# Kernel tuning notes

Hardware: AMD Instinct MI355X
Metric: run time of the kernel (lower is better)

Reference implementation:

```python
import jax, jax.numpy as jnp
import numpy as np

D_IN = 1024
D_OUT = 1024
NUM_HEADS = 16
HEAD_DIM = D_OUT // NUM_HEADS


def setup_inputs() -> dict:
    key = jax.random.key(0)
    k_x, k_q, k_k, k_v, k_o, k_ob = jax.random.split(key, 6)
    s_in = 1.0 / np.sqrt(D_IN)
    s_out = 1.0 / np.sqrt(D_OUT)
    return {
        "x": jax.random.normal(k_x, (2, 2048, D_IN), dtype=jnp.float32),
        "W_q": jax.random.uniform(k_q, (D_IN, D_OUT), minval=-s_in, maxval=s_in, dtype=jnp.float32),
        "W_k": jax.random.uniform(k_k, (D_IN, D_OUT), minval=-s_in, maxval=s_in, dtype=jnp.float32),
        "W_v": jax.random.uniform(k_v, (D_IN, D_OUT), minval=-s_in, maxval=s_in, dtype=jnp.float32),
        "W_out": jax.random.uniform(k_o, (D_OUT, D_OUT), minval=-s_out, maxval=s_out, dtype=jnp.float32),
        "b_out": jax.random.uniform(k_ob, (D_OUT,), minval=-s_out, maxval=s_out, dtype=jnp.float32),
    }


def reference(x, W_q, W_k, W_v, W_out, b_out):
    b, t, _ = x.shape
    # projections (qkv_bias=False)
    q = (x @ W_q).reshape(b, t, NUM_HEADS, HEAD_DIM).transpose(0, 2, 1, 3)  # [b,h,t,d]
    k = (x @ W_k).reshape(b, t, NUM_HEADS, HEAD_DIM).transpose(0, 2, 1, 3)
    v = (x @ W_v).reshape(b, t, NUM_HEADS, HEAD_DIM).transpose(0, 2, 1, 3)
    scale = 1.0 / np.sqrt(HEAD_DIM).astype(np.float32)
    scores = jnp.einsum("bhqd,bhkd->bhqk", q, k) * scale  # [b,h,t,t]
    causal = jnp.triu(jnp.ones((t, t), dtype=bool), k=1)
    scores = jnp.where(causal, -jnp.inf, scores)
    weights = jax.nn.softmax(scores, axis=-1)
    # dropout p=0.0 -> identity
    context = jnp.einsum("bhqk,bhkd->bhqd", weights, v)
    context = context.transpose(0, 2, 1, 3).reshape(b, t, D_OUT)
    return context @ W_out + b_out
```

## Files before the change

### kernel.cpp

```cpp
#include <hip/hip_runtime.h>
#include <hip/hip_bf16.h>

#define B_  2
#define T_  2048
#define D_  1024
#define H_  16
#define DH_ 64
#define M_  (B_*T_)

typedef _Float16 f16;
typedef __attribute__((ext_vector_type(4))) _Float16 f16x4;
typedef __attribute__((ext_vector_type(8))) _Float16 f16x8;
typedef __attribute__((ext_vector_type(4))) float f32x4;

#define GLOAD_LDS(gp, lp) __builtin_amdgcn_global_load_lds( \
    (const __attribute__((address_space(1))) void*)(gp),    \
    (__attribute__((address_space(3))) void*)(lp), 16, 0, 0)

__global__ void prep(const float* __restrict__ x,
                     const float* __restrict__ wq, const float* __restrict__ wk,
                     const float* __restrict__ wv, const float* __restrict__ wo,
                     f16* __restrict__ xb, f16* __restrict__ wqkvT, f16* __restrict__ woutT) {
  __shared__ float tile[32][33];
  const int bid = blockIdx.x;
  if (bid < 2048) {
    size_t i = ((size_t)bid * 256 + threadIdx.x) * 8;
    float4 a = *(const float4*)(x + i);
    float4 b = *(const float4*)(x + i + 4);
    f16x8 o;
    o[0]=(f16)a.x; o[1]=(f16)a.y; o[2]=(f16)a.z; o[3]=(f16)a.w;
    o[4]=(f16)b.x; o[5]=(f16)b.y; o[6]=(f16)b.z; o[7]=(f16)b.w;
    *(f16x8*)(xb + i) = o;
  } else {
    const int b2 = bid - 2048;
    const int j = b2 >> 10, rem = b2 & 1023;
    const float* src = (j==0)?wq:(j==1)?wk:(j==2)?wv:wo;
    f16* dst = (j<3) ? (wqkvT + (size_t)j*D_*D_) : woutT;
    const int n0 = (rem & 31)*32, k0 = (rem >> 5)*32;
    const int tx = threadIdx.x & 31, ty = threadIdx.x >> 5;
    #pragma unroll
    for (int i=0;i<32;i+=8)
      tile[ty+i][tx] = src[(size_t)(k0+ty+i)*D_ + n0+tx];
    __syncthreads();
    #pragma unroll
    for (int i=0;i<32;i+=8)
      dst[(size_t)(n0+ty+i)*D_ + k0+tx] = (f16)tile[tx][ty+i];
  }
}

__launch_bounds__(256, 2)
__global__ void qkv_gemm(const f16* __restrict__ xb, const f16* __restrict__ wT,
                         f16* __restrict__ Qp, f16* __restrict__ Kp, f16* __restrict__ Vtp) {
  const int fid = blockIdx.x;
  const int g = fid & 7, r = fid >> 3;
  const int m0 = ((((r & 3) << 3) | g)) * 128;
  const int n0 = ((r >> 2) & 7) * 128;
  const int j  = r >> 5;
  const f16* B0 = wT + (size_t)j * D_ * D_;
  __shared__ alignas(16) char smem[65536];
  f16* AsF = (f16*)smem;
  f16* BsF = AsF + 2*128*64;
  const int tid = threadIdx.x;
  const int lane = tid & 63, wave = tid >> 6;
  const int ln = lane & 15, quad = lane >> 4;
  const int wm = wave >> 1, wn = wave & 1;

  f32x4 acc[4][4];
  #pragma unroll
  for (int a=0;a<4;++a)
    #pragma unroll
    for (int b=0;b<4;++b) acc[a][b] = f32x4{0.f,0.f,0.f,0.f};

  const bool swapped = (j < 2);
  const int slot_row[4] = { (0*256+tid)>>3, (1*256+tid)>>3, (2*256+tid)>>3, (3*256+tid)>>3 };

  #pragma unroll
  for (int p = 0; p < 4; ++p) {
    int slot = p*256 + tid;
    int row  = slot_row[p];
    int c    = (slot & 7) ^ (row & 7);
    GLOAD_LDS(xb + (size_t)(m0+row)*D_ + c*8, AsF + (size_t)slot*8);
    GLOAD_LDS(B0 + (size_t)(n0+row)*D_ + c*8, BsF + (size_t)slot*8);
  }
  __syncthreads();

  for (int it = 0; it < 16; ++it) {
    const f16* Ac = AsF + (it & 1)*8192;
    const f16* Bc = BsF + (it & 1)*8192;
    if (it < 15) {
      const int k1 = (it + 1) * 64;
      f16* An = AsF + ((it + 1) & 1)*8192;
      f16* Bn = BsF + ((it + 1) & 1)*8192;
      #pragma unroll
      for (int p = 0; p < 4; ++p) {
        int slot = p*256 + tid;
        int row  = slot_row[p];
        int c    = (slot & 7) ^ (row & 7);
        GLOAD_LDS(xb + (size_t)(m0+row)*D_ + k1 + c*8, An + (size_t)slot*8);
        GLOAD_LDS(B0 + (size_t)(n0+row)*D_ + k1 + c*8, Bn + (size_t)slot*8);
      }
    }
    #pragma unroll
    for (int ks = 0; ks < 2; ++ks) {
      const int cb = ((ks*4 + quad) ^ (ln & 7)) * 8;
      f16x8 af[4], bf[4];
      #pragma unroll
      for (int mt = 0; mt < 4; ++mt)
        af[mt] = *(const f16x8*)(Ac + (size_t)(wm*64 + mt*16 + ln)*64 + cb);
      #pragma unroll
      for (int nt = 0; nt < 4; ++nt)
        bf[nt] = *(const f16x8*)(Bc + (size_t)(wn*64 + nt*16 + ln)*64 + cb);
      if (swapped) {
        #pragma unroll
        for (int nt = 0; nt < 4; ++nt)
          #pragma unroll
          for (int mt = 0; mt < 4; ++mt)
            acc[nt][mt] = __builtin_amdgcn_mfma_f32_16x16x32_f16(bf[nt], af[mt], acc[nt][mt], 0, 0, 0);
      } else {
        #pragma unroll
        for (int mt = 0; mt < 4; ++mt)
          #pragma unroll
          for (int nt = 0; nt < 4; ++nt)
            acc[mt][nt] = __builtin_amdgcn_mfma_f32_16x16x32_f16(af[mt], bf[nt], acc[mt][nt], 0, 0, 0);
      }
    }
    __syncthreads();
  }

  if (swapped) {
    const float scale = (j == 0) ? (0.125f * 1.44269504088896f) : 1.0f;
    f16* dstB = (j == 0) ? Qp : Kp;
    #pragma unroll
    for (int nt = 0; nt < 4; ++nt)
      #pragma unroll
      for (int mt = 0; mt < 4; ++mt) {
        int gm = m0 + wm*64 + mt*16 + ln;
        int gn = n0 + wn*64 + nt*16 + quad*4;
        int bb = gm >> 11, t = gm & (T_-1);
        int h  = gn >> 6,  dd = gn & (DH_-1);
        f16x4 v;
        #pragma unroll
        for (int rr = 0; rr < 4; ++rr) v[rr] = (f16)(acc[nt][mt][rr] * scale);
        *(f16x4*)&dstB[((((size_t)bb*H_ + h)*T_ + t)*DH_) + dd] = v;
      }
  } else {
    f16* VtS = (f16*)smem;
    #pragma unroll
    for (int mt = 0; mt < 4; ++mt)
      #pragma unroll
      for (int nt = 0; nt < 4; ++nt) {
        f16x4 v;
        v[0]=(f16)acc[mt][nt][0]; v[1]=(f16)acc[mt][nt][1];
        v[2]=(f16)acc[mt][nt][2]; v[3]=(f16)acc[mt][nt][3];
        *(f16x4*)&VtS[(size_t)(wn*64 + nt*16 + ln)*136 + wm*64 + mt*16 + quad*4] = v;
      }
    __syncthreads();
    int dd_loc = tid >> 1, half = tid & 1;
    int gn = n0 + dd_loc, h = gn >> 6, dd = gn & (DH_-1);
    int bb = m0 >> 11, tb = (m0 & (T_-1)) + half*64;
    f16* dst = Vtp + ((size_t)(bb*H_ + h)*DH_ + dd)*T_ + tb;
    const f16* src = VtS + (size_t)dd_loc*136 + half*64;
    #pragma unroll
    for (int u = 0; u < 8; ++u)
      *(uint4*)(dst + u*8) = *(const uint4*)(src + u*8);
  }
}

__launch_bounds__(256, 3)
__global__ void flash(const f16* __restrict__ Qp, const f16* __restrict__ Kp,
                      const f16* __restrict__ Vtp, f16* __restrict__ ctx) {
  const int fid = blockIdx.x;
  const int bh = fid & 31;
  const int qt = 31 - (fid >> 5);
  const int b = bh >> 4, h = bh & (H_-1);
  const f16* Kh = Kp  + (size_t)bh * T_ * DH_;
  const f16* Vh = Vtp + (size_t)bh * DH_ * T_;
  const f16* Qh = Qp  + (size_t)bh * T_ * DH_;
  const int tid = threadIdx.x, lane = tid & 63, w = tid >> 6;
  const int ln = lane & 15, quad = lane >> 4;

  __shared__ alignas(16) char smem[32768];
  f16* Ks = (f16*)smem;
  f16* Vs = (f16*)(smem + 16384);

  f16x8 qf[4][2];
  #pragma unroll
  for (int g = 0; g < 4; ++g)
    #pragma unroll
    for (int ks = 0; ks < 2; ++ks)
      qf[g][ks] = *(const f16x8*)&Qh[(size_t)(qt*64 + g*16 + ln)*DH_ + ks*32 + quad*8];

  f32x4 o[4][4];
  #pragma unroll
  for (int dt = 0; dt < 4; ++dt)
    #pragma unroll
    for (int g = 0; g < 4; ++g) o[dt][g] = f32x4{0.f,0.f,0.f,0.f};
  float lp[4] = {0.f, 0.f, 0.f, 0.f};

  #pragma unroll
  for (int i = 0; i < 2; ++i) {
    int slot = i*256 + tid;
    int row  = slot >> 3;
    int c    = (slot & 7) ^ (row & 7);
    GLOAD_LDS(Kh + (size_t)row*DH_ + c*8, Ks + (size_t)slot*8);
    GLOAD_LDS(Vh + (size_t)row*T_  + c*8, Vs + (size_t)slot*8);
  }
  __syncthreads();

  for (int it = 0; it <= qt; ++it) {
    const f16* Kc = Ks + (it & 1)*4096;
    const f16* Vc = Vs + (it & 1)*4096;
    if (it < qt) {
      const int kv1 = (it + 1)*64;
      f16* Kn = Ks + ((it + 1) & 1)*4096;
      f16* Vn = Vs + ((it + 1) & 1)*4096;
      #pragma unroll
      for (int i = 0; i < 2; ++i) {
        int slot = i*256 + tid;
        int row  = slot >> 3;
        int c    = (slot & 7) ^ (row & 7);
        GLOAD_LDS(Kh + (size_t)(kv1 + row)*DH_ + c*8, Kn + (size_t)slot*8);
        GLOAD_LDS(Vh + (size_t)row*T_ + kv1 + c*8,    Vn + (size_t)slot*8);
      }
    }

    f32x4 s[4];
    #pragma unroll
    for (int g = 0; g < 4; ++g) s[g] = f32x4{0.f,0.f,0.f,0.f};
    #pragma unroll
    for (int ks = 0; ks < 2; ++ks) {
      f16x8 kx = *(const f16x8*)(Kc + (size_t)(w*16 + ln)*64 + (((ks*4 + quad) ^ (ln & 7))*8));
      #pragma unroll
      for (int g = 0; g < 4; ++g)
        s[g] = __builtin_amdgcn_mfma_f32_16x16x32_f16(kx, qf[g][ks], s[g], 0, 0, 0);
    }

    if (it == qt) {
      #pragma unroll
      for (int g = 0; g < 4; ++g)
        #pragma unroll
        for (int rr = 0; rr < 4; ++rr)
          if (w*16 + quad*4 + rr > g*16 + ln) s[g][rr] = -INFINITY;
    }

    f16x4 pb[4];
    #pragma unroll
    for (int g = 0; g < 4; ++g) {
      #pragma unroll
      for (int rr = 0; rr < 4; ++rr) {
        float pe = __builtin_amdgcn_exp2f(s[g][rr]);
        lp[g] += pe;
        pb[g][rr] = (f16)pe;
      }
    }

    #pragma unroll
    for (int dt = 0; dt < 4; ++dt) {
      f16x4 vf = *(const f16x4*)(Vc + (size_t)(dt*16 + ln)*64
                   + (((2*w + (quad >> 1)) ^ (ln & 7))*8) + (quad & 1)*4);
      #pragma unroll
      for (int g = 0; g < 4; ++g)
        o[dt][g] = __builtin_amdgcn_mfma_f32_16x16x16f16(vf, pb[g], o[dt][g], 0, 0, 0);
    }
    __syncthreads();
  }

  #pragma unroll
  for (int g = 0; g < 4; ++g) {
    lp[g] += __shfl_xor(lp[g], 16, 64);
    lp[g] += __shfl_xor(lp[g], 32, 64);
  }

  float* buf = (float*)smem;
  #define WR_PART() do {                                                        \
    _Pragma("unroll")                                                           \
    for (int dt = 0; dt < 4; ++dt)                                              \
      _Pragma("unroll")                                                         \
      for (int g = 0; g < 4; ++g)                                               \
        *(f32x4*)&buf[(size_t)(g*16 + ln)*68 + dt*16 + quad*4] = o[dt][g];      \
    if (quad == 0) {                                                            \
      _Pragma("unroll")                                                         \
      for (int g = 0; g < 4; ++g) buf[64*68 + g*16 + ln] = lp[g];               \
    }                                                                           \
  } while (0)
  #define ACC_PART() do {                                                       \
    _Pragma("unroll")                                                           \
    for (int dt = 0; dt < 4; ++dt)                                              \
      _Pragma("unroll")                                                         \
      for (int g = 0; g < 4; ++g) {                                             \
        f32x4 v = *(const f32x4*)&buf[(size_t)(g*16 + ln)*68 + dt*16 + quad*4]; \
        o[dt][g][0] += v[0]; o[dt][g][1] += v[1];                               \
        o[dt][g][2] += v[2]; o[dt][g][3] += v[3];                               \
      }                                                                         \
    _Pragma("unroll")                                                           \
    for (int g = 0; g < 4; ++g) lp[g] += buf[64*68 + g*16 + ln];                \
  } while (0)

  if (w == 1) WR_PART();
  __syncthreads();
  if (w == 0) ACC_PART();
  __syncthreads();
  if (w == 2) WR_PART();
  __syncthreads();
  if (w == 0) ACC_PART();
  __syncthreads();
  if (w == 3) WR_PART();
  __syncthreads();
  if (w == 0) ACC_PART();
  __syncthreads();
  if (w == 0) WR_PART();
  __syncthreads();

  {
    const int q  = tid >> 2;
    const int dc = (tid & 3) << 4;
    const float linv = 1.0f / buf[64*68 + q];
    const float* src = &buf[(size_t)q*68 + dc];
    f16x8 o0, o1;
    #pragma unroll
    for (int jj = 0; jj < 8; ++jj) {
      o0[jj] = (f16)(src[jj] * linv);
      o1[jj] = (f16)(src[8 + jj] * linv);
    }
    f16* dst = &ctx[(size_t)(b*T_ + qt*64 + q)*D_ + h*DH_ + dc];
    *(f16x8*)dst       = o0;
    *(f16x8*)(dst + 8) = o1;
  }
  #undef WR_PART
  #undef ACC_PART
}

__launch_bounds__(256, 2)
__global__ void out_gemm(const f16* __restrict__ ctx, const f16* __restrict__ woT,
                         const float* __restrict__ bo, float* __restrict__ out) {
  const int fid = blockIdx.x;
  const int g = fid & 7, r = fid >> 3;
  const int m0 = ((((r & 3) << 3) | g)) * 128;
  const int n0 = (r >> 2) * 128;
  __shared__ alignas(16) f16 smem[4*128*64];
  f16* AsF = smem;
  f16* BsF = AsF + 2*128*64;
  const int tid = threadIdx.x;
  const int lane = tid & 63, wave = tid >> 6;
  const int ln = lane & 15, quad = lane >> 4;
  const int wm = wave >> 1, wn = wave & 1;

  f32x4 acc[4][4];
  #pragma unroll
  for (int a=0;a<4;++a)
    #pragma unroll
    for (int b=0;b<4;++b) acc[a][b] = f32x4{0.f,0.f,0.f,0.f};

  #pragma unroll
  for (int p = 0; p < 4; ++p) {
    int slot = p*256 + tid;
    int row  = slot >> 3;
    int c    = (slot & 7) ^ (row & 7);
    GLOAD_LDS(ctx + (size_t)(m0+row)*D_ + c*8, AsF + (size_t)slot*8);
    GLOAD_LDS(woT + (size_t)(n0+row)*D_ + c*8, BsF + (size_t)slot*8);
  }
  __syncthreads();

  for (int it = 0; it < 16; ++it) {
    const f16* Ac = AsF + (it & 1)*8192;
    const f16* Bc = BsF + (it & 1)*8192;
    if (it < 15) {
      const int k1 = (it + 1) * 64;
      f16* An = AsF + ((it + 1) & 1)*8192;
      f16* Bn = BsF + ((it + 1) & 1)*8192;
      #pragma unroll
      for (int p = 0; p < 4; ++p) {
        int slot = p*256 + tid;
        int row  = slot >> 3;
        int c    = (slot & 7) ^ (row & 7);
        GLOAD_LDS(ctx + (size_t)(m0+row)*D_ + k1 + c*8, An + (size_t)slot*8);
        GLOAD_LDS(woT + (size_t)(n0+row)*D_ + k1 + c*8, Bn + (size_t)slot*8);
      }
    }
    #pragma unroll
    for (int ks = 0; ks < 2; ++ks) {
      const int cb = ((ks*4 + quad) ^ (ln & 7)) * 8;
      f16x8 af[4], bf[4];
      #pragma unroll
      for (int mt = 0; mt < 4; ++mt)
        af[mt] = *(const f16x8*)(Ac + (size_t)(wm*64 + mt*16 + ln)*64 + cb);
      #pragma unroll
      for (int nt = 0; nt < 4; ++nt)
        bf[nt] = *(const f16x8*)(Bc + (size_t)(wn*64 + nt*16 + ln)*64 + cb);
      #pragma unroll
      for (int nt = 0; nt < 4; ++nt)
        #pragma unroll
        for (int mt = 0; mt < 4; ++mt)
          acc[nt][mt] = __builtin_amdgcn_mfma_f32_16x16x32_f16(bf[nt], af[mt], acc[nt][mt], 0, 0, 0);
    }
    __syncthreads();
  }

  #pragma unroll
  for (int nt = 0; nt < 4; ++nt) {
    int gn = n0 + wn*64 + nt*16 + quad*4;
    float4 bv = *(const float4*)&bo[gn];
    #pragma unroll
    for (int mt = 0; mt < 4; ++mt) {
      int gm = m0 + wm*64 + mt*16 + ln;
      float4 v;
      v.x = acc[nt][mt][0] + bv.x;
      v.y = acc[nt][mt][1] + bv.y;
      v.z = acc[nt][mt][2] + bv.z;
      v.w = acc[nt][mt][3] + bv.w;
      *(float4*)&out[(size_t)gm*D_ + gn] = v;
    }
  }
}

extern "C" void kernel_launch(void* const* d_in, const int* in_sizes, int n_in,
                              void* d_out, int out_size, void* d_ws, size_t ws_size,
                              hipStream_t stream) {
  const float* x  = (const float*)d_in[0];
  const float* wq = (const float*)d_in[1];
  const float* wk = (const float*)d_in[2];
  const float* wv = (const float*)d_in[3];
  const float* wo = (const float*)d_in[4];
  const float* bo = (const float*)d_in[5];
  float* out = (float*)d_out;

  f16* ws    = (f16*)d_ws;
  f16* xb    = ws;
  f16* wqkvT = xb    + (size_t)M_*D_;
  f16* woutT = wqkvT + (size_t)3*D_*D_;
  f16* Qb    = woutT + (size_t)D_*D_;
  f16* Kb    = Qb    + (size_t)M_*D_;
  f16* Vb    = Kb    + (size_t)M_*D_;
  f16* ctx   = Vb    + (size_t)M_*D_;

  prep<<<6144, 256, 0, stream>>>(x, wq, wk, wv, wo, xb, wqkvT, woutT);
  qkv_gemm<<<768, 256, 0, stream>>>(xb, wqkvT, Qb, Kb, Vb);
  flash<<<1024, 256, 0, stream>>>(Qb, Kb, Vb, ctx);
  out_gemm<<<256, 256, 0, stream>>>(ctx, woutT, bo, out);
}
```

Baseline: 167.5 us.

## Triple-buffer K/V tiles in flash attention with vmcnt-based waits

Moves the flash attention K/V staging from double to triple buffering, prefetching two tiles ahead. The full __syncthreads per iteration becomes a partial s_waitcnt vmcnt(4) plus a barrier, so loads for the next tile can stay in flight while the current tile is computed. This adds 16KB of LDS per block, which may cut occupancy under the 3-blocks-per-SM launch bound. Near the end it issues redundant clamped loads of the last tile to keep the vmcnt accounting uniform.

```diff
diff --git a/kernel.cpp b/kernel.cpp
--- a/kernel.cpp
+++ b/kernel.cpp
@@ -179,9 +179,23 @@
   const int tid = threadIdx.x, lane = tid & 63, w = tid >> 6;
   const int ln = lane & 15, quad = lane >> 4;
 
-  __shared__ alignas(16) char smem[32768];
+  __shared__ alignas(16) char smem[49152];
   f16* Ks = (f16*)smem;
-  f16* Vs = (f16*)(smem + 16384);
+  f16* Vs = (f16*)(smem + 24576);
+
+  #define STAGE_KV(tt, bi) do {                                              \
+    const int kvr_ = (tt)*64;                                                \
+    _Pragma("unroll")                                                        \
+    for (int i_ = 0; i_ < 2; ++i_) {                                         \
+      int slot_ = i_*256 + tid;                                              \
+      int row_  = slot_ >> 3;                                                \
+      int c_    = (slot_ & 7) ^ (row_ & 7);                                  \
+      GLOAD_LDS(Kh + (size_t)(kvr_ + row_)*DH_ + c_*8,                       \
+                Ks + (size_t)(bi)*4096 + (size_t)slot_*8);                   \
+      GLOAD_LDS(Vh + (size_t)row_*T_ + kvr_ + c_*8,                          \
+                Vs + (size_t)(bi)*4096 + (size_t)slot_*8);                   \
+    }                                                                        \
+  } while (0)
 
   f16x8 qf[4][2];
   #pragma unroll
@@ -197,32 +211,19 @@
     for (int g = 0; g < 4; ++g) o[dt][g] = f32x4{0.f,0.f,0.f,0.f};
   float lp[4] = {0.f, 0.f, 0.f, 0.f};
 
-  #pragma unroll
-  for (int i = 0; i < 2; ++i) {
-    int slot = i*256 + tid;
-    int row  = slot >> 3;
-    int c    = (slot & 7) ^ (row & 7);
-    GLOAD_LDS(Kh + (size_t)row*DH_ + c*8, Ks + (size_t)slot*8);
-    GLOAD_LDS(Vh + (size_t)row*T_  + c*8, Vs + (size_t)slot*8);
-  }
-  __syncthreads();
+  STAGE_KV(0, 0);
+  { const int t1 = (qt >= 1) ? 1 : qt; STAGE_KV(t1, 1); }
 
   for (int it = 0; it <= qt; ++it) {
-    const f16* Kc = Ks + (it & 1)*4096;
-    const f16* Vc = Vs + (it & 1)*4096;
-    if (it < qt) {
-      const int kv1 = (it + 1)*64;
-      f16* Kn = Ks + ((it + 1) & 1)*4096;
-      f16* Vn = Vs + ((it + 1) & 1)*4096;
-      #pragma unroll
-      for (int i = 0; i < 2; ++i) {
-        int slot = i*256 + tid;
-        int row  = slot >> 3;
-        int c    = (slot & 7) ^ (row & 7);
-        GLOAD_LDS(Kh + (size_t)(kv1 + row)*DH_ + c*8, Kn + (size_t)slot*8);
-        GLOAD_LDS(Vh + (size_t)row*T_ + kv1 + c*8,    Vn + (size_t)slot*8);
-      }
-    }
+    const int cur = it % 3;
+    const f16* Kc = Ks + (size_t)cur*4096;
+    const f16* Vc = Vs + (size_t)cur*4096;
+
+    asm volatile("s_waitcnt vmcnt(4)" ::: "memory");
+    __builtin_amdgcn_s_barrier();
+    asm volatile("" ::: "memory");
+
+    { const int tn = (it + 2 <= qt) ? (it + 2) : qt; STAGE_KV(tn, (it + 2) % 3); }
 
     f32x4 s[4];
     #pragma unroll
@@ -262,8 +263,11 @@
       for (int g = 0; g < 4; ++g)
         o[dt][g] = __builtin_amdgcn_mfma_f32_16x16x16f16(vf, pb[g], o[dt][g], 0, 0, 0);
     }
-    __syncthreads();
-  }
+  }
+
+  asm volatile("s_waitcnt vmcnt(0)" ::: "memory");
+  __builtin_amdgcn_s_barrier();
+  asm volatile("" ::: "memory");
 
   #pragma unroll
   for (int g = 0; g < 4; ++g) {
@@ -328,6 +332,7 @@
   }
   #undef WR_PART
   #undef ACC_PART
+  #undef STAGE_KV
 }
 
 __launch_bounds__(256, 2)
```

Result: no change. 166.2 us (-0.8%).

## Retile QKV GEMM to 256x256 blocks with 512 threads and BK=32

Applied to the files above, without the earlier changes.

The QKV projection GEMM now uses 256x256 output tiles per block with 8 waves and a K-step of 32, using a new XOR-swizzled LDS layout and a single barrier per iteration with explicit vmcnt waits. MFMA sections are wrapped in s_setprio. The V-transpose epilogue no longer goes through LDS and writes 4-element vectors straight to the transposed layout. The aim is more operand reuse per LDS byte and fewer barriers. The risks are that 192 blocks underfill the 256 CUs, and that the V stores become narrower and strided.

```diff
diff --git a/kernel.cpp b/kernel.cpp
--- a/kernel.cpp
+++ b/kernel.cpp
@@ -48,84 +48,92 @@
   }
 }
 
-__launch_bounds__(256, 2)
+__launch_bounds__(512, 2)
 __global__ void qkv_gemm(const f16* __restrict__ xb, const f16* __restrict__ wT,
                          f16* __restrict__ Qp, f16* __restrict__ Kp, f16* __restrict__ Vtp) {
   const int fid = blockIdx.x;
-  const int g = fid & 7, r = fid >> 3;
-  const int m0 = ((((r & 3) << 3) | g)) * 128;
-  const int n0 = ((r >> 2) & 7) * 128;
-  const int j  = r >> 5;
-  const f16* B0 = wT + (size_t)j * D_ * D_;
-  __shared__ alignas(16) char smem[65536];
-  f16* AsF = (f16*)smem;
-  f16* BsF = AsF + 2*128*64;
+  const int mb = fid & 15, nf = fid >> 4;
+  const int m0 = mb * 256;
+  const int n0f = nf * 256;
+  const int j  = n0f >> 10;
+  const int n0 = n0f & 1023;
+  const f16* A0 = xb + (size_t)m0*D_;
+  const f16* B0 = wT + (size_t)j*D_*D_ + (size_t)n0*D_;
+  __shared__ alignas(16) f16 smem[4*256*32];
+  f16* As = smem;
+  f16* Bs = smem + 2*256*32;
   const int tid = threadIdx.x;
   const int lane = tid & 63, wave = tid >> 6;
   const int ln = lane & 15, quad = lane >> 4;
-  const int wm = wave >> 1, wn = wave & 1;
-
-  f32x4 acc[4][4];
+  const int wm = wave >> 2, wn = wave & 3;
+
+  const bool swapped = (j < 2);
+
+  f32x4 acc[4][8];
   #pragma unroll
   for (int a=0;a<4;++a)
     #pragma unroll
-    for (int b=0;b<4;++b) acc[a][b] = f32x4{0.f,0.f,0.f,0.f};
-
-  const bool swapped = (j < 2);
-  const int slot_row[4] = { (0*256+tid)>>3, (1*256+tid)>>3, (2*256+tid)>>3, (3*256+tid)>>3 };
-
-  #pragma unroll
-  for (int p = 0; p < 4; ++p) {
-    int slot = p*256 + tid;
-    int row  = slot_row[p];
-    int c    = (slot & 7) ^ (row & 7);
-    GLOAD_LDS(xb + (size_t)(m0+row)*D_ + c*8, AsF + (size_t)slot*8);
-    GLOAD_LDS(B0 + (size_t)(n0+row)*D_ + c*8, BsF + (size_t)slot*8);
-  }
-  __syncthreads();
-
-  for (int it = 0; it < 16; ++it) {
-    const f16* Ac = AsF + (it & 1)*8192;
-    const f16* Bc = BsF + (it & 1)*8192;
-    if (it < 15) {
-      const int k1 = (it + 1) * 64;
-      f16* An = AsF + ((it + 1) & 1)*8192;
-      f16* Bn = BsF + ((it + 1) & 1)*8192;
-      #pragma unroll
-      for (int p = 0; p < 4; ++p) {
-        int slot = p*256 + tid;
-        int row  = slot_row[p];
-        int c    = (slot & 7) ^ (row & 7);
-        GLOAD_LDS(xb + (size_t)(m0+row)*D_ + k1 + c*8, An + (size_t)slot*8);
-        GLOAD_LDS(B0 + (size_t)(n0+row)*D_ + k1 + c*8, Bn + (size_t)slot*8);
-      }
-    }
-    #pragma unroll
-    for (int ks = 0; ks < 2; ++ks) {
-      const int cb = ((ks*4 + quad) ^ (ln & 7)) * 8;
-      f16x8 af[4], bf[4];
-      #pragma unroll
-      for (int mt = 0; mt < 4; ++mt)
-        af[mt] = *(const f16x8*)(Ac + (size_t)(wm*64 + mt*16 + ln)*64 + cb);
+    for (int b=0;b<8;++b) acc[a][b] = f32x4{0.f,0.f,0.f,0.f};
+
+  #define STAGE(tt, bi) do {                                                  \
+    const int k0_ = (tt)*32;                                                  \
+    _Pragma("unroll")                                                         \
+    for (int p_ = 0; p_ < 2; ++p_) {                                          \
+      int slot_ = p_*512 + tid;                                               \
+      int pr_ = slot_ >> 3, pb_ = slot_ & 7;                                  \
+      int ob_ = pb_ ^ (pr_ & 7);                                              \
+      int r_  = pr_*2 + (ob_ >> 2);                                           \
+      int cb_ = ob_ & 3;                                                      \
+      GLOAD_LDS(A0 + (size_t)r_*D_ + k0_ + cb_*8,                             \
+                As + (size_t)(bi)*8192 + (size_t)slot_*8);                    \
+      GLOAD_LDS(B0 + (size_t)r_*D_ + k0_ + cb_*8,                             \
+                Bs + (size_t)(bi)*8192 + (size_t)slot_*8);                    \
+    }                                                                         \
+  } while (0)
+
+  STAGE(0, 0);
+
+  for (int t = 0; t < 32; ++t) {
+    asm volatile("s_waitcnt vmcnt(0)" ::: "memory");
+    __builtin_amdgcn_s_barrier();
+    if (t < 31) STAGE(t + 1, (t + 1) & 1);
+
+    const f16* Ac = As + (size_t)(t & 1)*8192;
+    const f16* Bc = Bs + (size_t)(t & 1)*8192;
+
+    f16x8 af[8], bf[4];
+    #pragma unroll
+    for (int mt = 0; mt < 8; ++mt) {
+      int r  = wm*128 + mt*16 + ln;
+      int pr = r >> 1;
+      int pb = (((r & 1) << 2) | quad) ^ (pr & 7);
+      af[mt] = *(const f16x8*)(Ac + (size_t)pr*64 + pb*8);
+    }
+    #pragma unroll
+    for (int nt = 0; nt < 4; ++nt) {
+      int r  = wn*64 + nt*16 + ln;
+      int pr = r >> 1;
+      int pb = (((r & 1) << 2) | quad) ^ (pr & 7);
+      bf[nt] = *(const f16x8*)(Bc + (size_t)pr*64 + pb*8);
+    }
+
+    __builtin_amdgcn_s_setprio(1);
+    if (swapped) {
       #pragma unroll
       for (int nt = 0; nt < 4; ++nt)
-        bf[nt] = *(const f16x8*)(Bc + (size_t)(wn*64 + nt*16 + ln)*64 + cb);
-      if (swapped) {
         #pragma unroll
-        for (int nt = 0; nt < 4; ++nt)
-          #pragma unroll
-          for (int mt = 0; mt < 4; ++mt)
-            acc[nt][mt] = __builtin_amdgcn_mfma_f32_16x16x32_f16(bf[nt], af[mt], acc[nt][mt], 0, 0, 0);
-      } else {
+        for (int mt = 0; mt < 8; ++mt)
+          acc[nt][mt] = __builtin_amdgcn_mfma_f32_16x16x32_f16(bf[nt], af[mt], acc[nt][mt], 0, 0, 0);
+    } else {
+      #pragma unroll
+      for (int nt = 0; nt < 4; ++nt)
         #pragma unroll
-        for (int mt = 0; mt < 4; ++mt)
-          #pragma unroll
-          for (int nt = 0; nt < 4; ++nt)
-            acc[mt][nt] = __builtin_amdgcn_mfma_f32_16x16x32_f16(af[mt], bf[nt], acc[mt][nt], 0, 0, 0);
-      }
-    }
-    __syncthreads();
-  }
+        for (int mt = 0; mt < 8; ++mt)
+          acc[nt][mt] = __builtin_amdgcn_mfma_f32_16x16x32_f16(af[mt], bf[nt], acc[nt][mt], 0, 0, 0);
+    }
+    __builtin_amdgcn_s_setprio(0);
+  }
+  #undef STAGE
 
   if (swapped) {
     const float scale = (j == 0) ? (0.125f * 1.44269504088896f) : 1.0f;
@@ -133,36 +141,30 @@
     #pragma unroll
     for (int nt = 0; nt < 4; ++nt)
       #pragma unroll
-      for (int mt = 0; mt < 4; ++mt) {
-        int gm = m0 + wm*64 + mt*16 + ln;
-        int gn = n0 + wn*64 + nt*16 + quad*4;
-        int bb = gm >> 11, t = gm & (T_-1);
-        int h  = gn >> 6,  dd = gn & (DH_-1);
+      for (int mt = 0; mt < 8; ++mt) {
+        int gm  = m0 + wm*128 + mt*16 + ln;
+        int gnl = n0 + wn*64 + nt*16 + quad*4;
+        int bb = gm >> 11, tt = gm & (T_-1);
+        int h  = gnl >> 6, dd = gnl & (DH_-1);
         f16x4 v;
         #pragma unroll
         for (int rr = 0; rr < 4; ++rr) v[rr] = (f16)(acc[nt][mt][rr] * scale);
-        *(f16x4*)&dstB[((((size_t)bb*H_ + h)*T_ + t)*DH_) + dd] = v;
+        *(f16x4*)&dstB[((((size_t)bb*H_ + h)*T_ + tt)*DH_) + dd] = v;
       }
   } else {
-    f16* VtS = (f16*)smem;
-    #pragma unroll
-    for (int mt = 0; mt < 4; ++mt)
-      #pragma unroll
-      for (int nt = 0; nt < 4; ++nt) {
+    #pragma unroll
+    for (int nt = 0; nt < 4; ++nt)
+      #pragma unroll
+      for (int mt = 0; mt < 8; ++mt) {
+        int gm  = m0 + wm*128 + mt*16 + quad*4;
+        int gnl = n0 + wn*64 + nt*16 + ln;
+        int bb = gm >> 11, tt = gm & (T_-1);
+        int h  = gnl >> 6, dd = gnl & (DH_-1);
         f16x4 v;
-        v[0]=(f16)acc[mt][nt][0]; v[1]=(f16)acc[mt][nt][1];
-        v[2]=(f16)acc[mt][nt][2]; v[3]=(f16)acc[mt][nt][3];
-        *(f16x4*)&VtS[(size_t)(wn*64 + nt*16 + ln)*136 + wm*64 + mt*16 + quad*4] = v;
+        v[0]=(f16)acc[nt][mt][0]; v[1]=(f16)acc[nt][mt][1];
+        v[2]=(f16)acc[nt][mt][2]; v[3]=(f16)acc[nt][mt][3];
+        *(f16x4*)&Vtp[((size_t)(bb*H_ + h)*DH_ + dd)*T_ + tt] = v;
       }
-    __syncthreads();
-    int dd_loc = tid >> 1, half = tid & 1;
-    int gn = n0 + dd_loc, h = gn >> 6, dd = gn & (DH_-1);
-    int bb = m0 >> 11, tb = (m0 & (T_-1)) + half*64;
-    f16* dst = Vtp + ((size_t)(bb*H_ + h)*DH_ + dd)*T_ + tb;
-    const f16* src = VtS + (size_t)dd_loc*136 + half*64;
-    #pragma unroll
-    for (int u = 0; u < 8; ++u)
-      *(uint4*)(dst + u*8) = *(const uint4*)(src + u*8);
   }
 }
 
@@ -434,7 +436,7 @@
   f16* ctx   = Vb    + (size_t)M_*D_;
 
   prep<<<6144, 256, 0, stream>>>(x, wq, wk, wv, wo, xb, wqkvT, woutT);
-  qkv_gemm<<<768, 256, 0, stream>>>(xb, wqkvT, Qb, Kb, Vb);
+  qkv_gemm<<<192, 512, 0, stream>>>(xb, wqkvT, Qb, Kb, Vb);
   flash<<<1024, 256, 0, stream>>>(Qb, Kb, Vb, ctx);
   out_gemm<<<256, 256, 0, stream>>>(ctx, woutT, bo, out);
 }
```

New measurement: 372.7 us. 123% more time.

## Single-buffer QKV GEMM LDS tiles to fit three blocks per CU

Applied to the files above, without the earlier changes.

Replaces the double-buffered LDS staging in the QKV projection GEMM with a single buffer, roughly halving shared memory per block, and raises the launch bound to three blocks per CU. The next K-tile is now loaded only after compute on the current tile finishes, with barriers on both sides, so loads no longer overlap MFMA work within a block. The intent is to hide that latency through higher occupancy across blocks instead, at the cost of tighter register limits and lost intra-block prefetch.

```diff
diff --git a/kernel.cpp b/kernel.cpp
--- a/kernel.cpp
+++ b/kernel.cpp
@@ -48,7 +48,7 @@
   }
 }
 
-__launch_bounds__(256, 2)
+__launch_bounds__(256, 3)
 __global__ void qkv_gemm(const f16* __restrict__ xb, const f16* __restrict__ wT,
                          f16* __restrict__ Qp, f16* __restrict__ Kp, f16* __restrict__ Vtp) {
   const int fid = blockIdx.x;
@@ -56,10 +56,11 @@
   const int m0 = ((((r & 3) << 3) | g)) * 128;
   const int n0 = ((r >> 2) & 7) * 128;
   const int j  = r >> 5;
-  const f16* B0 = wT + (size_t)j * D_ * D_;
-  __shared__ alignas(16) char smem[65536];
+  const f16* A0 = xb + (size_t)m0 * D_;
+  const f16* B0 = wT + (size_t)j * D_ * D_ + (size_t)n0 * D_;
+  __shared__ alignas(16) char smem[34816];
   f16* AsF = (f16*)smem;
-  f16* BsF = AsF + 2*128*64;
+  f16* BsF = AsF + 128*64;
   const int tid = threadIdx.x;
   const int lane = tid & 63, wave = tid >> 6;
   const int ln = lane & 15, quad = lane >> 4;
@@ -72,44 +73,33 @@
     for (int b=0;b<4;++b) acc[a][b] = f32x4{0.f,0.f,0.f,0.f};
 
   const bool swapped = (j < 2);
-  const int slot_row[4] = { (0*256+tid)>>3, (1*256+tid)>>3, (2*256+tid)>>3, (3*256+tid)>>3 };
-
-  #pragma unroll
-  for (int p = 0; p < 4; ++p) {
-    int slot = p*256 + tid;
-    int row  = slot_row[p];
-    int c    = (slot & 7) ^ (row & 7);
-    GLOAD_LDS(xb + (size_t)(m0+row)*D_ + c*8, AsF + (size_t)slot*8);
-    GLOAD_LDS(B0 + (size_t)(n0+row)*D_ + c*8, BsF + (size_t)slot*8);
-  }
-  __syncthreads();
+
+  #define STAGE(tt) do {                                                      \
+    const int k0_ = (tt)*64;                                                  \
+    _Pragma("unroll")                                                         \
+    for (int p_ = 0; p_ < 4; ++p_) {                                          \
+      int slot_ = p_*256 + tid;                                               \
+      int row_  = slot_ >> 3;                                                 \
+      int c_    = (slot_ & 7) ^ (row_ & 7);                                   \
+      GLOAD_LDS(A0 + (size_t)row_*D_ + k0_ + c_*8, AsF + (size_t)slot_*8);    \
+      GLOAD_LDS(B0 + (size_t)row_*D_ + k0_ + c_*8, BsF + (size_t)slot_*8);    \
+    }                                                                         \
+  } while (0)
+
+  STAGE(0);
 
   for (int it = 0; it < 16; ++it) {
-    const f16* Ac = AsF + (it & 1)*8192;
-    const f16* Bc = BsF + (it & 1)*8192;
-    if (it < 15) {
-      const int k1 = (it + 1) * 64;
-      f16* An = AsF + ((it + 1) & 1)*8192;
-      f16* Bn = BsF + ((it + 1) & 1)*8192;
-      #pragma unroll
-      for (int p = 0; p < 4; ++p) {
-        int slot = p*256 + tid;
-        int row  = slot_row[p];
-        int c    = (slot & 7) ^ (row & 7);
-        GLOAD_LDS(xb + (size_t)(m0+row)*D_ + k1 + c*8, An + (size_t)slot*8);
-        GLOAD_LDS(B0 + (size_t)(n0+row)*D_ + k1 + c*8, Bn + (size_t)slot*8);
-      }
-    }
+    __syncthreads();
     #pragma unroll
     for (int ks = 0; ks < 2; ++ks) {
       const int cb = ((ks*4 + quad) ^ (ln & 7)) * 8;
       f16x8 af[4], bf[4];
       #pragma unroll
       for (int mt = 0; mt < 4; ++mt)
-        af[mt] = *(const f16x8*)(Ac + (size_t)(wm*64 + mt*16 + ln)*64 + cb);
+        af[mt] = *(const f16x8*)(AsF + (size_t)(wm*64 + mt*16 + ln)*64 + cb);
       #pragma unroll
       for (int nt = 0; nt < 4; ++nt)
-        bf[nt] = *(const f16x8*)(Bc + (size_t)(wn*64 + nt*16 + ln)*64 + cb);
+        bf[nt] = *(const f16x8*)(BsF + (size_t)(wn*64 + nt*16 + ln)*64 + cb);
       if (swapped) {
         #pragma unroll
         for (int nt = 0; nt < 4; ++nt)
@@ -125,7 +115,9 @@
       }
     }
     __syncthreads();
-  }
+    if (it < 15) STAGE(it + 1);
+  }
+  #undef STAGE
 
   if (swapped) {
     const float scale = (j == 0) ? (0.125f * 1.44269504088896f) : 1.0f;
```

Result: slower. 203.2 us (+21.3%).
